# Kernel optimization log

Measured on AMD Instinct MI355X. Metric: run time of the kernel, lower is better.

Reference implementation:

```python
import jax, jax.numpy as jnp
import numpy as np

GRID = 32
N = GRID * GRID
KTOP = 256          # max off-diagonal points kept per diagram (rest are diagonal, zero cost)
SINK_ITERS = 150
_idx = np.arange(N).reshape(GRID, GRID)
_EU = np.concatenate([_idx[:, :-1].ravel(), _idx[:-1, :].ravel()]).astype(np.int32)
_EV = np.concatenate([_idx[:, 1:].ravel(), _idx[1:, :].ravel()]).astype(np.int32)
E = _EU.shape[0]  # 1984 grid edges (4-connectivity, V-construction cubical complex)


def _h0_pairs(v):
    """0-dim persistence pairs of the sublevel filtration of pixel values v [N].
    Kruskal/union-find with the elder rule; trivial edges emit diagonal (w, w) pairs."""
    eu, ev = jnp.asarray(_EU), jnp.asarray(_EV)
    w = jnp.maximum(v[eu], v[ev])
    order = jnp.argsort(w)

    @jax.checkpoint
    def step(state, edge):
        parent, birth = state
        u, vv, wgt = edge
        for _ in range(10):              # pointer jumping: full compression (2^10 >= N)
            parent = parent[parent]
        ru, rv = parent[u], parent[vv]
        bu, bv = birth[ru], birth[rv]
        merge = ru != rv
        u_older = bu <= bv
        older = jnp.where(u_older, ru, rv)
        younger = jnp.where(u_older, rv, ru)
        pb = jnp.where(merge, jnp.maximum(bu, bv), wgt)   # younger component dies
        parent = parent.at[younger].set(jnp.where(merge, older, younger))
        birth = birth.at[older].set(jnp.minimum(bu, bv))
        return (parent, birth), (pb, wgt)

    init = (jnp.arange(N, dtype=jnp.int32), v)
    _, (bs, ds) = jax.lax.scan(step, init, (eu[order], ev[order], w[order]))
    return bs, ds


def _diagrams(img):
    """img [GRID,GRID] -> (b0, d0, b1, d1), each [KTOP]. H1 via superlevel H0 duality."""
    v = img.reshape(-1)
    b0, d0 = _h0_pairs(v)
    b0 = jnp.concatenate([b0, v.min()[None]])   # essential H0 class: (min, max)
    d0 = jnp.concatenate([d0, v.max()[None]])
    nb, nd = _h0_pairs(-v)                       # superlevel-set H0 (essential dropped)
    b1, d1 = -nd, -nb

    def topk(b, d):
        _, i = jax.lax.top_k(d - b, KTOP)        # keep most persistent points
        return b[i], d[i]

    return (*topk(b0, d0), *topk(b1, d1))


def _wasserstein(ab, ad, bb, bd):
    """Entropic 1-Wasserstein between diagrams with L-inf ground metric and diagonal slots."""
    K = ab.shape[0]
    Pa = jnp.stack([ab, ad], -1)
    Pb = jnp.stack([bb, bd], -1)
    Mpp = jnp.max(jnp.abs(Pa[:, None, :] - Pb[None, :, :]), -1)  # [K,K]
    da = 0.5 * (ad - ab)                       # L-inf distance of a-points to diagonal
    db = 0.5 * (bd - bb)
    C = jnp.block([[Mpp, jnp.broadcast_to(da[:, None], (K, K))],
                   [jnp.broadcast_to(db[None, :], (K, K)), jnp.zeros((K, K), ab.dtype)]])
    eps = 0.02 * jnp.maximum(jnp.max(C), 1e-6)

    def it(_, fg):
        f, g = fg
        f = -eps * jax.nn.logsumexp((g[None, :] - C) / eps, axis=1)
        g = -eps * jax.nn.logsumexp((f[:, None] - C) / eps, axis=0)
        return f, g

    f, g = jax.lax.fori_loop(0, SINK_ITERS, it, (jnp.zeros(2 * K), jnp.zeros(2 * K)))
    P = jnp.exp((f[:, None] + g[None, :] - C) / eps)
    return jnp.sum(P * C)


def setup_inputs() -> dict:
    key = jax.random.key(0)
    kx, ky = jax.random.split(key)
    x = jax.random.normal(kx, (4, 4, 256, 256), dtype=jnp.float32)
    y = jax.random.randint(ky, (4, 1, 256, 256), 0, 4)
    return {"x": x, "y": y}


def reference(x, y):
    B, C, H, W = x.shape
    x = jax.nn.softmax(x, axis=1)                               # apply_nonlin
    y_oh = (y == jnp.arange(C)[None, :, None, None]).astype(x.dtype)  # scatter_ one-hot
    kh, kw = H // GRID, W // GRID

    def pool(t):  # adaptive_avg_pool2d to (32, 32)
        b, c = t.shape[:2]
        return t.reshape(b, c, GRID, kh, GRID, kw).mean((3, 5))

    mx = pool(x[:, 1:]).reshape(-1, GRID, GRID)  # drop background channel
    my = pool(y_oh[:, 1:]).reshape(-1, GRID, GRID)
    dx = jax.vmap(_diagrams)(mx)
    dy = jax.vmap(_diagrams)(my)
    w0 = jax.vmap(_wasserstein)(dx[0], dx[1], dy[0], dy[1])
    w1 = jax.vmap(_wasserstein)(dx[2], dx[3], dy[2], dy[3])
    return (jnp.sum(w0) + jnp.sum(w1)) / B
```

## Files before the change

### kernel.cpp

```cpp
#include <hip/hip_runtime.h>
#include <cmath>

#define NPIX 1024
#define NEDGE 1984
#define NPAD 2048
#define KTOP 256
#define NITER 150

typedef __attribute__((ext_vector_type(8))) short bf16x8_t;
typedef __attribute__((ext_vector_type(4))) float f32x4_t;

__device__ __forceinline__ unsigned bf_rne(float x) {
    unsigned b = __float_as_uint(x);
    return (b + 0x7fffu + ((b >> 16) & 1u)) >> 16;
}
__device__ __forceinline__ float rcpf(float x) { return __builtin_amdgcn_rcpf(x); }

template<int CTRL>
__device__ __forceinline__ float dppf(float x) {
    return __int_as_float(__builtin_amdgcn_update_dpp(
        __float_as_int(x), __float_as_int(x), CTRL, 0xF, 0xF, false));
}
__device__ __forceinline__ void wave_red2(float& s, float& m) {
    s += dppf<0x121>(s); m = fminf(m, dppf<0x121>(m));
    s += dppf<0x122>(s); m = fminf(m, dppf<0x122>(m));
    s += dppf<0x124>(s); m = fminf(m, dppf<0x124>(m));
    s += dppf<0x128>(s); m = fminf(m, dppf<0x128>(m));
    s += __int_as_float(__builtin_amdgcn_ds_swizzle(__float_as_int(s), 0x401F));
    m = fminf(m, __int_as_float(__builtin_amdgcn_ds_swizzle(__float_as_int(m), 0x401F)));
    float s0 = __int_as_float(__builtin_amdgcn_readlane(__float_as_int(s), 0));
    float s1 = __int_as_float(__builtin_amdgcn_readlane(__float_as_int(s), 32));
    s = s0 + s1;
    float m0 = __int_as_float(__builtin_amdgcn_readlane(__float_as_int(m), 0));
    float m1 = __int_as_float(__builtin_amdgcn_readlane(__float_as_int(m), 32));
    m = fminf(m0, m1);
}

__device__ __forceinline__ float min8v(const float* a) {
    float4 x0 = *(const float4*)a, x1 = *(const float4*)(a + 4);
    return fminf(fminf(fminf(x0.x, x0.y), fminf(x0.z, x0.w)),
                 fminf(fminf(x1.x, x1.y), fminf(x1.z, x1.w)));
}
__device__ __forceinline__ float sum8v(const float* a) {
    float4 x0 = *(const float4*)a, x1 = *(const float4*)(a + 4);
    return ((x0.x + x0.y) + (x0.z + x0.w)) + ((x1.x + x1.y) + (x1.z + x1.w));
}

__global__ __launch_bounds__(256) void pool_kernel(const float* __restrict__ x,
                                                   const int* __restrict__ y,
                                                   float* __restrict__ pooled) {
    int blk = blockIdx.x;
    int img = blk >> 2;
    int cell = ((blk & 3) << 8) | threadIdx.x;
    int gi = cell >> 5, gj = cell & 31;
    const float L2E = 1.4426950408889634f;
    float acc = 0.f;
    if (img < 12) {
        int b = img / 3, c = img % 3 + 1;
        const float* xb = x + (size_t)b * 262144 + (size_t)gi * 2048 + gj * 8;
        for (int pi = 0; pi < 8; ++pi) {
            const float* xr = xb + pi * 256;
            #pragma unroll
            for (int ph = 0; ph < 2; ++ph) {
                float4 c0 = *(const float4*)(xr + ph * 4);
                float4 c1 = *(const float4*)(xr + ph * 4 + 65536);
                float4 c2 = *(const float4*)(xr + ph * 4 + 131072);
                float4 c3 = *(const float4*)(xr + ph * 4 + 196608);
                const float* f0 = (const float*)&c0;
                const float* f1 = (const float*)&c1;
                const float* f2 = (const float*)&c2;
                const float* f3 = (const float*)&c3;
                #pragma unroll
                for (int k = 0; k < 4; ++k) {
                    float e0 = exp2f(f0[k] * L2E), e1 = exp2f(f1[k] * L2E);
                    float e2 = exp2f(f2[k] * L2E), e3 = exp2f(f3[k] * L2E);
                    float ec = (c == 1) ? e1 : (c == 2) ? e2 : e3;
                    acc += ec / (e0 + e1 + e2 + e3);
                }
            }
        }
    } else {
        int tt = img - 12;
        int b = tt / 3, c = tt % 3 + 1;
        const int* yb = y + (size_t)b * 65536 + (size_t)gi * 2048 + gj * 8;
        int cnt = 0;
        for (int pi = 0; pi < 8; ++pi) {
            const int* yr = yb + pi * 256;
            #pragma unroll
            for (int pj = 0; pj < 8; ++pj) cnt += (yr[pj] == c) ? 1 : 0;
        }
        acc = (float)cnt;
    }
    pooled[img * NPIX + cell] = acc * (1.f / 64.f);
}

__device__ __forceinline__ void cex(unsigned long long& a, unsigned long long& b, bool up) {
    if ((a > b) == up) { unsigned long long t = a; a = b; b = t; }
}
__device__ void bitonic2048_reg(unsigned long long* keys, int tid, bool asc) {
    int i0 = tid << 2;
    for (int k = 2; k <= NPAD; k <<= 1) {
        for (int j = k >> 1; j >= 4; j >>= 1) {
            #pragma unroll
            for (int rep = 0; rep < 4; ++rep) {
                int ii = tid + rep * 512;
                int l = ii ^ j;
                if (l > ii) {
                    unsigned long long a = keys[ii], b = keys[l];
                    bool up = (((ii & k) == 0) == asc);
                    if ((a > b) == up) { keys[ii] = b; keys[l] = a; }
                }
            }
            __syncthreads();
        }
        unsigned long long e0 = keys[i0], e1 = keys[i0 + 1], e2 = keys[i0 + 2], e3 = keys[i0 + 3];
        bool upq = (((i0 & k) == 0) == asc);
        if (k >= 4) {
            cex(e0, e2, upq); cex(e1, e3, upq);
            cex(e0, e1, upq); cex(e2, e3, upq);
        } else {
            cex(e0, e1, asc);
            cex(e2, e3, !asc);
        }
        keys[i0] = e0; keys[i0 + 1] = e1; keys[i0 + 2] = e2; keys[i0 + 3] = e3;
        __syncthreads();
    }
}

__global__ __launch_bounds__(512) void diag_kernel(const float* __restrict__ pooled,
                                                   float* __restrict__ diag) {
    __shared__ float v_[NPIX];
    __shared__ unsigned long long keys[NPAD];
    __shared__ unsigned long long PB[NPIX];
    __shared__ unsigned euv[NPAD];
    __shared__ unsigned long long pbd[NEDGE];
    __shared__ unsigned long long snap[132];
    __shared__ unsigned long long clist[132];
    __shared__ unsigned long long smask[2];
    __shared__ unsigned claimA[NPIX];
    __shared__ unsigned histAll[2048];
    __shared__ float redA[8], redB[8];
    __shared__ float svmin, svmax;
    __shared__ unsigned long long s_prefix, s_T;
    __shared__ unsigned s_need, s_done, s_outcnt, s_ncon;

    int run = blockIdx.x;
    int img = run >> 1, filt = run & 1;
    int tid = threadIdx.x;
    int wv = tid >> 6;
    const float* m = pooled + img * NPIX;

    for (int i = tid; i < NPIX; i += 512) {
        float val = m[i];
        v_[i] = filt ? -val : val;
    }
    __syncthreads();
    float mn = INFINITY, mx = -INFINITY;
    for (int i = tid; i < NPIX; i += 512) { float vv = v_[i]; mn = fminf(mn, vv); mx = fmaxf(mx, vv); }
    for (int o = 32; o; o >>= 1) { mn = fminf(mn, __shfl_xor(mn, o)); mx = fmaxf(mx, __shfl_xor(mx, o)); }
    if ((tid & 63) == 0) { redA[wv] = mn; redB[wv] = mx; }
    __syncthreads();
    if (tid == 0) {
        float a = INFINITY, b = -INFINITY;
        for (int i2 = 0; i2 < 8; ++i2) { a = fminf(a, redA[i2]); b = fmaxf(b, redB[i2]); }
        svmin = a; svmax = b;
    }
    for (int e = tid; e < NPAD; e += 512) {
        unsigned long long key;
        unsigned uv = 0;
        if (e < NEDGE) {
            int u, vv;
            if (e < 992) { int r = e / 31; u = e + r; vv = u + 1; }
            else         { u = e - 992;   vv = u + 32; }
            float w = fmaxf(v_[u], v_[vv]);
            unsigned int bw = __float_as_uint(w);
            bw = (bw & 0x80000000u) ? ~bw : (bw | 0x80000000u);
            key = ((unsigned long long)bw << 11) | (unsigned int)e;
            uv = (unsigned)u | ((unsigned)vv << 16);
        } else key = ~0ULL;
        keys[e] = key;
        euv[e] = uv;
    }
    for (int i = tid; i < NPIX; i += 512)
        PB[i] = ((unsigned long long)__float_as_uint(v_[i]) << 32) | (unsigned)i;
    __syncthreads();
    bitonic2048_reg(keys, tid, true);

    unsigned* PBlo = (unsigned*)PB;
    for (int base = 0; base < NEDGE; base += 128) {
        for (int i = tid; i < NPIX; i += 512) claimA[i] = 0xFFFFFFFFu;
        if (base) {
            for (int rd = 0; rd < 4; ++rd) {
                for (int i = tid; i < NPIX; i += 512) {
                    unsigned pp = PBlo[2 * i];
                    unsigned gg = PBlo[2 * pp];
                    PBlo[2 * i] = gg;
                }
            }
        }
        __syncthreads();
        int bend = (base + 128 < NEDGE) ? base + 128 : NEDGE;
        int bcnt = bend - base;
        if (tid < bcnt) {
            int kk = base + tid;
            unsigned long long key = keys[kk];
            int e = (int)(key & 2047ULL);
            unsigned bw = (unsigned)(key >> 11);
            unsigned uv = euv[e];
            int ra = (int)(uv & 0xffffu), rb = (int)(uv >> 16);
            unsigned pp = PBlo[2 * ra];
            while (pp != (unsigned)ra) { ra = (int)pp; pp = PBlo[2 * ra]; }
            unsigned p2 = PBlo[2 * rb];
            while (p2 != (unsigned)rb) { rb = (int)p2; p2 = PBlo[2 * rb]; }
            if (ra == rb) {
                unsigned wb = (bw & 0x80000000u) ? (bw & 0x7fffffffu) : ~bw;
                pbd[kk] = (unsigned long long)wb | ((unsigned long long)wb << 32);
                snap[tid] = 0ULL;
            } else {
                snap[tid] = ((unsigned long long)bw << 22)
                          | ((unsigned)(ra + 1) << 11) | (unsigned)(rb + 1);
                atomicMin(&claimA[ra], (unsigned)tid);
                atomicMin(&claimA[rb], (unsigned)tid);
            }
        }
        __syncthreads();
        bool pend = false;
        if (tid < bcnt) {
            unsigned long long sc = snap[tid];
            if ((unsigned)(sc & 0x3FFFFFu)) {
                int ra = (int)((sc >> 11) & 0x7FFu) - 1;
                int rb = (int)(sc & 0x7FFu) - 1;
                if (claimA[ra] == (unsigned)tid && claimA[rb] == (unsigned)tid) {
                    unsigned ob = (unsigned)(sc >> 22);
                    float w = __uint_as_float((ob & 0x80000000u) ? (ob & 0x7fffffffu) : ~ob);
                    float bu = v_[ra], bv = v_[rb];
                    bool uo = (bu <= bv);
                    int older = uo ? ra : rb;
                    int younger = uo ? rb : ra;
                    PBlo[2 * younger] = (unsigned)older;
                    float pb_ = fmaxf(bu, bv);
                    pbd[base + tid] = (unsigned long long)__float_as_uint(pb_)
                                    | ((unsigned long long)__float_as_uint(w) << 32);
                } else pend = true;
            }
        }
        unsigned long long bmask = __ballot(pend);
        if ((tid & 63) == 0 && wv < 2) smask[wv] = bmask;
        __syncthreads();
        if (pend) {
            int lane = tid & 63;
            int pos = __popcll(bmask & ((1ULL << lane) - 1ULL))
                    + (wv ? __popcll(smask[0]) : 0);
            clist[pos] = snap[tid] | ((unsigned long long)tid << 54);
        }
        if (tid == 256) {
            unsigned n = (unsigned)(__popcll(smask[0]) + __popcll(smask[1]));
            s_ncon = n;
            clist[n] = 0ULL;
        }
        __syncthreads();
        if (tid == 0) {
            int n = (int)s_ncon;
            unsigned long long sc = clist[0];
            for (int i = 0; i < n; ++i) {
                unsigned long long sn = clist[i + 1];
                int slot = (int)(sc >> 54);
                unsigned ob = (unsigned)((sc >> 22) & 0xFFFFFFFFu);
                float w = __uint_as_float((ob & 0x80000000u) ? (ob & 0x7fffffffu) : ~ob);
                int a = (int)((sc >> 11) & 0x7FFu) - 1;
                int b = (int)(sc & 0x7FFu) - 1;
                unsigned long long qa = PB[a], qb = PB[b];
                int pa = (int)(unsigned)qa, pb = (int)(unsigned)qb;
                while (pa != a || pb != b) {
                    if (pa != a) {
                        unsigned long long na = PB[pa];
                        int ga = (int)(unsigned)na;
                        PBlo[2 * a] = (unsigned)ga;
                        a = pa; pa = ga; qa = na;
                    }
                    if (pb != b) {
                        unsigned long long nb = PB[pb];
                        int gb = (int)(unsigned)nb;
                        PBlo[2 * b] = (unsigned)gb;
                        b = pb; pb = gb; qb = nb;
                    }
                }
                float pb_, pd_;
                if (a != b) {
                    float bu = __uint_as_float((unsigned)(qa >> 32));
                    float bv = __uint_as_float((unsigned)(qb >> 32));
                    bool uo = (bu <= bv);
                    int older = uo ? a : b;
                    int younger = uo ? b : a;
                    pb_ = fmaxf(bu, bv); pd_ = w;
                    PBlo[2 * younger] = (unsigned)older;
                } else { pb_ = w; pd_ = w; }
                pbd[base + slot] = (unsigned long long)__float_as_uint(pb_)
                                 | ((unsigned long long)__float_as_uint(pd_) << 32);
                sc = sn;
            }
        }
        __syncthreads();
    }

    int count = filt ? NEDGE : (NEDGE + 1);
    for (int k = tid; k < NPAD; k += 512) {
        unsigned long long key = 0ULL;
        if (k < count) {
            float pers;
            if (k < NEDGE) {
                unsigned long long pd2 = pbd[k];
                pers = __uint_as_float((unsigned)(pd2 >> 32)) - __uint_as_float((unsigned)pd2);
            } else pers = svmax - svmin;
            key = ((unsigned long long)__float_as_uint(pers) << 32) | (unsigned int)(2047 - k);
        }
        keys[k] = key;
    }
    if (tid == 0) { s_prefix = 0ULL; s_T = 0ULL; s_need = KTOP; s_done = 0; s_outcnt = 0; }
    __syncthreads();

    for (int rnd = 0; rnd < 8; ++rnd) {
        for (int i = tid; i < 2048; i += 512) histAll[i] = 0;
        __syncthreads();
        if (!s_done) {
            int shift = 56 - 8 * rnd;
            unsigned long long pref = s_prefix;
            for (int k = tid; k < NPAD; k += 512) {
                unsigned long long key = keys[k];
                bool act = (rnd == 0) || ((key >> (shift + 8)) == (pref >> (shift + 8)));
                if (act) atomicAdd(&histAll[wv * 256 + (unsigned)((key >> shift) & 255ULL)], 1u);
            }
        }
        __syncthreads();
        if (wv == 0) {
            if (!s_done) {
                int l64 = tid;
                int shift = 56 - 8 * rnd;
                unsigned c0 = 0, c1 = 0, c2 = 0, c3 = 0;
                #pragma unroll
                for (int cp = 0; cp < 8; ++cp) {
                    const unsigned* h = histAll + cp * 256 + 4 * l64;
                    c0 += h[0]; c1 += h[1]; c2 += h[2]; c3 += h[3];
                }
                unsigned s3 = c3, s2 = c2 + s3, s1 = c1 + s2, s0 = c0 + s1;
                unsigned acc2 = s0;
                #pragma unroll
                for (int o = 1; o < 64; o <<= 1) {
                    unsigned v2 = __shfl_down(acc2, o);
                    if (l64 + o < 64) acc2 += v2;
                }
                unsigned above = acc2 - s0;
                unsigned Sn[5] = {above + s0, above + s1, above + s2, above + s3, above};
                unsigned need = s_need;
                #pragma unroll
                for (int q2 = 0; q2 < 4; ++q2) {
                    if (Sn[q2] >= need && Sn[q2 + 1] < need) {
                        unsigned bstar = 4 * l64 + q2;
                        if (Sn[q2] == need) {
                            s_T = s_prefix | ((unsigned long long)bstar << shift);
                            s_done = 1;
                        } else {
                            s_prefix = s_prefix | ((unsigned long long)bstar << shift);
                            s_need = need - Sn[q2 + 1];
                        }
                    }
                }
            }
        }
        __syncthreads();
    }

    {
        unsigned long long T = s_T;
        for (int k = tid; k < NPAD; k += 512) {
            unsigned long long key = keys[k];
            if (key >= T && key != 0ULL) {
                int pos = (int)atomicAdd(&s_outcnt, 1u);
                int kk = 2047 - (int)(key & 0xffffffffULL);
                float b_, d_;
                if (kk < NEDGE) {
                    unsigned long long pd2 = pbd[kk];
                    b_ = __uint_as_float((unsigned)pd2);
                    d_ = __uint_as_float((unsigned)(pd2 >> 32));
                } else { b_ = svmin; d_ = svmax; }
                float ob, od;
                if (!filt) { ob = b_;  od = d_;  }
                else       { ob = -d_; od = -b_; }
                diag[((img * 4) + filt * 2 + 0) * KTOP + pos] = ob;
                diag[((img * 4) + filt * 2 + 1) * KTOP + pos] = od;
            }
        }
    }
}

__global__ __launch_bounds__(512) void sink_kernel(const float* __restrict__ diag,
                                                   float* __restrict__ wres) {
    __shared__ float2 sPA[KTOP], sPB[KTOP];
    __shared__ float sda[KTOP], sdb[KTOP];
    __shared__ float swa[KTOP], swb[KTOP];
    __shared__ __align__(16) unsigned ug_bf[128];
    __shared__ __align__(16) unsigned uf_bf[128];
    __shared__ __align__(16) float uf32[KTOP], ug32[KTOP];
    __shared__ __align__(16) float minF[8], accTF[8], minG[8], accTG[8];
    __shared__ __align__(16) float pm[8];
    __shared__ float s_sig, s_invsig;

    int p = blockIdx.x;
    int img = p % 12, dim = p / 12;
    int t = threadIdx.x;
    int lane = t & 63, w = t >> 6;
    int lr = lane & 15, lg = lane >> 4;
    int r = t >> 1, q = t & 1, jb = q * 128;

    const float* ab  = diag + ((img * 4) + dim * 2) * KTOP;
    const float* ad  = ab + KTOP;
    const float* bbp = diag + (((12 + img) * 4) + dim * 2) * KTOP;
    const float* bdp = bbp + KTOP;

    if (t < KTOP) {
        float a0 = ab[t], a1 = ad[t];
        float b0 = bbp[t], b1 = bdp[t];
        sPA[t] = make_float2(a0, a1);
        sPB[t] = make_float2(b0, b1);
        sda[t] = 0.5f * (a1 - a0);
        sdb[t] = 0.5f * (b1 - b0);
    }
    if (t < 128) ug_bf[t] = 0x3F803F80u;
    __syncthreads();

    {
        float2 A = sPA[r];
        float lmax = 0.f;
        for (int jj = 0; jj < 128; ++jj) {
            float2 B = sPB[jb + jj];
            lmax = fmaxf(lmax, fmaxf(fabsf(A.x - B.x), fabsf(A.y - B.y)));
        }
        if (t < KTOP) lmax = fmaxf(lmax, fmaxf(sda[t], sdb[t]));
        for (int o = 32; o; o >>= 1) lmax = fmaxf(lmax, __shfl_xor(lmax, o));
        if (lane == 0) pm[w] = lmax;
    }
    __syncthreads();
    if (t == 0) {
        float mc = 0.f;
        for (int i = 0; i < 8; ++i) mc = fmaxf(mc, pm[i]);
        float eps = 0.02f * fmaxf(mc, 1e-6f);
        s_sig = 1.4426950408889634f / eps;
        s_invsig = eps * 0.6931471805599453f;
    }
    __syncthreads();
    {
        float sig = s_sig;
        if (t < KTOP) {
            float2 a2 = sPA[t], b2 = sPB[t];
            sPA[t] = make_float2(a2.x * sig, a2.y * sig);
            sPB[t] = make_float2(b2.x * sig, b2.y * sig);
            float da2 = sda[t] * sig, db2 = sdb[t] * sig;
            sda[t] = da2; sdb[t] = db2;
            swa[t] = exp2f(-da2); swb[t] = exp2f(-db2);
        }
    }
    __syncthreads();

    bf16x8_t KfA0[8], KfA1[8], KgA0[8], KgA1[8];
    {
        float2 Af0 = sPA[w * 32 + lr];
        float2 Af1 = sPA[w * 32 + 16 + lr];
        float2 Bg0 = sPB[w * 32 + lr];
        float2 Bg1 = sPB[w * 32 + 16 + lr];
        #pragma unroll
        for (int ks = 0; ks < 8; ++ks) {
            #pragma unroll
            for (int jj = 0; jj < 8; ++jj) {
                int b = ks * 32 + lg * 8 + jj;
                float2 Pb = sPB[b];
                KfA0[ks][jj] = (short)bf_rne(exp2f(-fmaxf(fabsf(Af0.x - Pb.x), fabsf(Af0.y - Pb.y))));
                KfA1[ks][jj] = (short)bf_rne(exp2f(-fmaxf(fabsf(Af1.x - Pb.x), fabsf(Af1.y - Pb.y))));
                float2 Pa = sPA[b];
                KgA0[ks][jj] = (short)bf_rne(exp2f(-fmaxf(fabsf(Pa.x - Bg0.x), fabsf(Pa.y - Bg0.y))));
                KgA1[ks][jj] = (short)bf_rne(exp2f(-fmaxf(fabsf(Pa.x - Bg1.x), fabsf(Pa.y - Bg1.y))));
            }
        }
    }
    float wa0[4], wa1[4], wb0[4], wb1[4];
    #pragma unroll
    for (int g2 = 0; g2 < 4; ++g2) {
        wa0[g2] = swa[w * 32 + lg * 4 + g2];
        wa1[g2] = swa[w * 32 + 16 + lg * 4 + g2];
        wb0[g2] = swb[w * 32 + lg * 4 + g2];
        wb1[g2] = swb[w * 32 + 16 + lg * 4 + g2];
    }

    float cg = 1.f, cf = 1.f, uG2s = 1.f, uF2s = 1.f;
    f32x4_t ugs0 = {1.f, 1.f, 1.f, 1.f}, ugs1 = {1.f, 1.f, 1.f, 1.f};
    f32x4_t ufs0 = {0.f, 0.f, 0.f, 0.f}, ufs1 = {0.f, 0.f, 0.f, 0.f};

    for (int it = 0; it < NITER; ++it) {
        if (it) {
            cg = min8v(minG);
            uG2s = rcpf(cf * (sum8v(accTG) + 256.f * uF2s));
        }
        {
            bf16x8_t Bf[8];
            #pragma unroll
            for (int ks = 0; ks < 8; ++ks) Bf[ks] = ((const bf16x8_t*)ug_bf)[ks * 4 + lg];
            f32x4_t a0 = {0.f, 0.f, 0.f, 0.f}, a1 = {0.f, 0.f, 0.f, 0.f};
            #pragma unroll
            for (int ks = 0; ks < 8; ++ks) {
                a0 = __builtin_amdgcn_mfma_f32_16x16x32_bf16(KfA0[ks], Bf[ks], a0, 0, 0, 0);
                a1 = __builtin_amdgcn_mfma_f32_16x16x32_bf16(KfA1[ks], Bf[ks], a1, 0, 0, 0);
            }
            float mv = INFINITY, tv = 0.f;
            #pragma unroll
            for (int g2 = 0; g2 < 4; ++g2) {
                float R0 = cg * (a0[g2] + 256.f * uG2s * wa0[g2]);
                float R1 = cg * (a1[g2] + 256.f * uG2s * wa1[g2]);
                ufs0[g2] = rcpf(R0); ufs1[g2] = rcpf(R1);
                mv = fminf(mv, fminf(R0, R1));
                tv += ugs0[g2] * wb0[g2] + ugs1[g2] * wb1[g2];
            }
            if (lr == 0) {
                uint2 v0, v1;
                v0.x = bf_rne(ufs0[0]) | (bf_rne(ufs0[1]) << 16);
                v0.y = bf_rne(ufs0[2]) | (bf_rne(ufs0[3]) << 16);
                v1.x = bf_rne(ufs1[0]) | (bf_rne(ufs1[1]) << 16);
                v1.y = bf_rne(ufs1[2]) | (bf_rne(ufs1[3]) << 16);
                ((uint2*)uf_bf)[w * 8 + lg] = v0;
                ((uint2*)uf_bf)[w * 8 + 4 + lg] = v1;
            }
            wave_red2(tv, mv);
            if (lane == 0) { accTF[w] = tv * 0.0625f; minF[w] = mv; }
        }
        __syncthreads();
        cf = min8v(minF);
        uF2s = rcpf(cg * (sum8v(accTF) + 256.f * uG2s));
        {
            bf16x8_t Bf[8];
            #pragma unroll
            for (int ks = 0; ks < 8; ++ks) Bf[ks] = ((const bf16x8_t*)uf_bf)[ks * 4 + lg];
            f32x4_t a0 = {0.f, 0.f, 0.f, 0.f}, a1 = {0.f, 0.f, 0.f, 0.f};
            #pragma unroll
            for (int ks = 0; ks < 8; ++ks) {
                a0 = __builtin_amdgcn_mfma_f32_16x16x32_bf16(KgA0[ks], Bf[ks], a0, 0, 0, 0);
                a1 = __builtin_amdgcn_mfma_f32_16x16x32_bf16(KgA1[ks], Bf[ks], a1, 0, 0, 0);
            }
            float mv = INFINITY, tv = 0.f;
            #pragma unroll
            for (int g2 = 0; g2 < 4; ++g2) {
                float Q0 = cf * (a0[g2] + 256.f * uF2s * wb0[g2]);
                float Q1 = cf * (a1[g2] + 256.f * uF2s * wb1[g2]);
                ugs0[g2] = rcpf(Q0); ugs1[g2] = rcpf(Q1);
                mv = fminf(mv, fminf(Q0, Q1));
                tv += ufs0[g2] * wa0[g2] + ufs1[g2] * wa1[g2];
            }
            if (lr == 0) {
                uint2 v0, v1;
                v0.x = bf_rne(ugs0[0]) | (bf_rne(ugs0[1]) << 16);
                v0.y = bf_rne(ugs0[2]) | (bf_rne(ugs0[3]) << 16);
                v1.x = bf_rne(ugs1[0]) | (bf_rne(ugs1[1]) << 16);
                v1.y = bf_rne(ugs1[2]) | (bf_rne(ugs1[3]) << 16);
                ((uint2*)ug_bf)[w * 8 + lg] = v0;
                ((uint2*)ug_bf)[w * 8 + 4 + lg] = v1;
            }
            wave_red2(tv, mv);
            if (lane == 0) { accTG[w] = tv * 0.0625f; minG[w] = mv; }
        }
        __syncthreads();
    }
    float uG2f = rcpf(cf * (sum8v(accTG) + 256.f * uF2s));
    if (lr == 0) {
        ((f32x4_t*)uf32)[w * 8 + lg] = ufs0;
        ((f32x4_t*)uf32)[w * 8 + 4 + lg] = ufs1;
        ((f32x4_t*)ug32)[w * 8 + lg] = ugs0;
        ((f32x4_t*)ug32)[w * 8 + 4 + lg] = ugs1;
    }
    __syncthreads();

    float accv = 0.f;
    {
        float2 Apt = sPA[r];
        float ufr = uf32[r];
        #pragma unroll 8
        for (int jj = 0; jj < 128; ++jj) {
            int j = jb + jj;
            float2 B = sPB[j];
            float Mh = fmaxf(fabsf(Apt.x - B.x), fabsf(Apt.y - B.y));
            float kv = __uint_as_float(bf_rne(exp2f(-Mh)) << 16);
            accv += ((ufr * kv) * ug32[j]) * Mh;
        }
        if (q == 0) accv += 256.f * ((ufr * swa[r]) * uG2f) * sda[r];
        else        accv += 256.f * ((uF2s * swb[r]) * ug32[r]) * sdb[r];
    }
    accv *= cf;
    for (int o = 32; o; o >>= 1) accv += __shfl_xor(accv, o);
    if (lane == 0) pm[w] = accv;
    __syncthreads();
    if (t == 0) {
        float tot = 0.f;
        for (int i = 0; i < 8; ++i) tot += pm[i];
        wres[p] = tot * s_invsig;
    }
}

__global__ void finalize_kernel(const float* __restrict__ wres, float* __restrict__ out) {
    if (threadIdx.x == 0) {
        float s = 0.f;
        for (int i = 0; i < 24; ++i) s += wres[i];
        out[0] = s * 0.25f;
    }
}

extern "C" void kernel_launch(void* const* d_in, const int* in_sizes, int n_in,
                              void* d_out, int out_size, void* d_ws, size_t ws_size,
                              hipStream_t stream) {
    const float* x = (const float*)d_in[0];
    const int* y = (const int*)d_in[1];
    float* ws = (float*)d_ws;
    float* pooled = ws;
    float* diag = pooled + 24 * NPIX;
    float* wres = diag + 24 * 4 * KTOP;

    pool_kernel<<<96, 256, 0, stream>>>(x, y, pooled);
    diag_kernel<<<48, 512, 0, stream>>>(pooled, diag);
    sink_kernel<<<24, 512, 0, stream>>>(diag, wres);
    finalize_kernel<<<1, 64, 0, stream>>>(wres, (float*)d_out);
}
```

Before: 767.8 us.

## Widen parallel union-find batches to 512 edges with multi-round claiming; split MFMA chains

The H0 union-find phase now processes 512 sorted edges per batch instead of 128. It runs up to three rounds of atomicMax-based root claiming, with root re-finding between rounds, before handing leftover conflicts to the serial single-thread fallback. This is meant to cut the number of batches and barriers and shrink the serial conflict loop. The cost is extra rounds and syncs per batch and possibly more conflicts per batch. Separately, the Sinkhorn MFMA accumulation is split into two independent accumulator chains to shorten the dependency latency.

```diff
diff --git a/kernel.cpp b/kernel.cpp
--- a/kernel.cpp
+++ b/kernel.cpp
@@ -134,9 +134,9 @@
     __shared__ unsigned long long PB[NPIX];
     __shared__ unsigned euv[NPAD];
     __shared__ unsigned long long pbd[NEDGE];
-    __shared__ unsigned long long snap[132];
-    __shared__ unsigned long long clist[132];
-    __shared__ unsigned long long smask[2];
+    __shared__ unsigned long long snap[516];
+    __shared__ unsigned long long clist[516];
+    __shared__ unsigned long long smask[8];
     __shared__ unsigned claimA[NPIX];
     __shared__ unsigned histAll[2048];
     __shared__ float redA[8], redB[8];
@@ -187,8 +187,8 @@
     bitonic2048_reg(keys, tid, true);
 
     unsigned* PBlo = (unsigned*)PB;
-    for (int base = 0; base < NEDGE; base += 128) {
-        for (int i = tid; i < NPIX; i += 512) claimA[i] = 0xFFFFFFFFu;
+    for (int base = 0; base < NEDGE; base += 512) {
+        for (int i = tid; i < NPIX; i += 512) claimA[i] = 0u;
         if (base) {
             for (int rd = 0; rd < 4; ++rd) {
                 for (int i = tid; i < NPIX; i += 512) {
@@ -199,8 +199,9 @@
             }
         }
         __syncthreads();
-        int bend = (base + 128 < NEDGE) ? base + 128 : NEDGE;
+        int bend = (base + 512 < NEDGE) ? base + 512 : NEDGE;
         int bcnt = bend - base;
+        bool pend = false;
         if (tid < bcnt) {
             int kk = base + tid;
             unsigned long long key = keys[kk];
@@ -219,18 +220,20 @@
             } else {
                 snap[tid] = ((unsigned long long)bw << 22)
                           | ((unsigned)(ra + 1) << 11) | (unsigned)(rb + 1);
-                atomicMin(&claimA[ra], (unsigned)tid);
-                atomicMin(&claimA[rb], (unsigned)tid);
-            }
-        }
-        __syncthreads();
-        bool pend = false;
-        if (tid < bcnt) {
-            unsigned long long sc = snap[tid];
-            if ((unsigned)(sc & 0x3FFFFFu)) {
+                unsigned tg = (1u << 12) | (unsigned)(511 - tid);
+                atomicMax(&claimA[ra], tg);
+                atomicMax(&claimA[rb], tg);
+                pend = true;
+            }
+        }
+        __syncthreads();
+        for (int rnd = 0; rnd < 3; ++rnd) {
+            if (pend) {
+                unsigned long long sc = snap[tid];
                 int ra = (int)((sc >> 11) & 0x7FFu) - 1;
                 int rb = (int)(sc & 0x7FFu) - 1;
-                if (claimA[ra] == (unsigned)tid && claimA[rb] == (unsigned)tid) {
+                unsigned tg = ((unsigned)(rnd + 1) << 12) | (unsigned)(511 - tid);
+                if (claimA[ra] == tg && claimA[rb] == tg) {
                     unsigned ob = (unsigned)(sc >> 22);
                     float w = __uint_as_float((ob & 0x80000000u) ? (ob & 0x7fffffffu) : ~ob);
                     float bu = v_[ra], bv = v_[rb];
@@ -241,20 +244,50 @@
                     float pb_ = fmaxf(bu, bv);
                     pbd[base + tid] = (unsigned long long)__float_as_uint(pb_)
                                     | ((unsigned long long)__float_as_uint(w) << 32);
-                } else pend = true;
+                    snap[tid] = 0ULL;
+                    pend = false;
+                }
+            }
+            __syncthreads();
+            if (rnd < 2) {
+                if (pend) {
+                    unsigned long long sc = snap[tid];
+                    int ra = (int)((sc >> 11) & 0x7FFu) - 1;
+                    int rb = (int)(sc & 0x7FFu) - 1;
+                    unsigned pp = PBlo[2 * ra];
+                    while (pp != (unsigned)ra) { ra = (int)pp; pp = PBlo[2 * ra]; }
+                    unsigned p2 = PBlo[2 * rb];
+                    while (p2 != (unsigned)rb) { rb = (int)p2; p2 = PBlo[2 * rb]; }
+                    if (ra == rb) {
+                        unsigned ob = (unsigned)(sc >> 22);
+                        unsigned wb2 = (ob & 0x80000000u) ? (ob & 0x7fffffffu) : ~ob;
+                        pbd[base + tid] = (unsigned long long)wb2
+                                        | ((unsigned long long)wb2 << 32);
+                        snap[tid] = 0ULL;
+                        pend = false;
+                    } else {
+                        snap[tid] = (sc & ~0x3FFFFFULL)
+                                  | ((unsigned)(ra + 1) << 11) | (unsigned)(rb + 1);
+                        unsigned tg = ((unsigned)(rnd + 2) << 12) | (unsigned)(511 - tid);
+                        atomicMax(&claimA[ra], tg);
+                        atomicMax(&claimA[rb], tg);
+                    }
+                }
+                __syncthreads();
             }
         }
         unsigned long long bmask = __ballot(pend);
-        if ((tid & 63) == 0 && wv < 2) smask[wv] = bmask;
+        if ((tid & 63) == 0) smask[wv] = bmask;
         __syncthreads();
         if (pend) {
             int lane = tid & 63;
-            int pos = __popcll(bmask & ((1ULL << lane) - 1ULL))
-                    + (wv ? __popcll(smask[0]) : 0);
+            int pos = __popcll(bmask & ((1ULL << lane) - 1ULL));
+            for (int w2 = 0; w2 < wv; ++w2) pos += __popcll(smask[w2]);
             clist[pos] = snap[tid] | ((unsigned long long)tid << 54);
         }
-        if (tid == 256) {
-            unsigned n = (unsigned)(__popcll(smask[0]) + __popcll(smask[1]));
+        if (tid == 0) {
+            unsigned n = 0;
+            for (int w2 = 0; w2 < 8; ++w2) n += (unsigned)__popcll(smask[w2]);
             s_ncon = n;
             clist[n] = 0ULL;
         }
@@ -504,11 +537,16 @@
             #pragma unroll
             for (int ks = 0; ks < 8; ++ks) Bf[ks] = ((const bf16x8_t*)ug_bf)[ks * 4 + lg];
             f32x4_t a0 = {0.f, 0.f, 0.f, 0.f}, a1 = {0.f, 0.f, 0.f, 0.f};
-            #pragma unroll
-            for (int ks = 0; ks < 8; ++ks) {
+            f32x4_t c0 = {0.f, 0.f, 0.f, 0.f}, c1 = {0.f, 0.f, 0.f, 0.f};
+            #pragma unroll
+            for (int ks = 0; ks < 4; ++ks) {
                 a0 = __builtin_amdgcn_mfma_f32_16x16x32_bf16(KfA0[ks], Bf[ks], a0, 0, 0, 0);
                 a1 = __builtin_amdgcn_mfma_f32_16x16x32_bf16(KfA1[ks], Bf[ks], a1, 0, 0, 0);
-            }
+                c0 = __builtin_amdgcn_mfma_f32_16x16x32_bf16(KfA0[ks + 4], Bf[ks + 4], c0, 0, 0, 0);
+                c1 = __builtin_amdgcn_mfma_f32_16x16x32_bf16(KfA1[ks + 4], Bf[ks + 4], c1, 0, 0, 0);
+            }
+            a0 = a0 + c0;
+            a1 = a1 + c1;
             float mv = INFINITY, tv = 0.f;
             #pragma unroll
             for (int g2 = 0; g2 < 4; ++g2) {
@@ -538,11 +576,16 @@
             #pragma unroll
             for (int ks = 0; ks < 8; ++ks) Bf[ks] = ((const bf16x8_t*)uf_bf)[ks * 4 + lg];
             f32x4_t a0 = {0.f, 0.f, 0.f, 0.f}, a1 = {0.f, 0.f, 0.f, 0.f};
-            #pragma unroll
-            for (int ks = 0; ks < 8; ++ks) {
+            f32x4_t c0 = {0.f, 0.f, 0.f, 0.f}, c1 = {0.f, 0.f, 0.f, 0.f};
+            #pragma unroll
+            for (int ks = 0; ks < 4; ++ks) {
                 a0 = __builtin_amdgcn_mfma_f32_16x16x32_bf16(KgA0[ks], Bf[ks], a0, 0, 0, 0);
                 a1 = __builtin_amdgcn_mfma_f32_16x16x32_bf16(KgA1[ks], Bf[ks], a1, 0, 0, 0);
-            }
+                c0 = __builtin_amdgcn_mfma_f32_16x16x32_bf16(KgA0[ks + 4], Bf[ks + 4], c0, 0, 0, 0);
+                c1 = __builtin_amdgcn_mfma_f32_16x16x32_bf16(KgA1[ks + 4], Bf[ks + 4], c1, 0, 0, 0);
+            }
+            a0 = a0 + c0;
+            a1 = a1 + c1;
             float mv = INFINITY, tv = 0.f;
             #pragma unroll
             for (int g2 = 0; g2 < 4; ++g2) {
```

New measurement: 764.6 us. About the same (-0.4%).
